# Optimization experiments

Hardware: AMD Instinct MI355X
Metric: run time of the kernel (lower is better)

Reference implementation:

```python
import jax, jax.numpy as jnp
import numpy as np
from jax import ops as jops

N = 20000          # nodes
E = 320000         # edges
IN_DIM = 16        # input_dim_features_extractor
HID = 64           # hidden_dim_features_extractor
HEADS = 4          # n_attention_heads
LAYERS = 2         # n_layers_features_extractor
NEG_SLOPE = 0.2    # DGL EGATConv leaky_relu slope


def setup_inputs() -> dict:
    key = jax.random.key(0)
    ks = jax.random.split(key, 16)
    s = lambda *sh: 1.0 / np.sqrt(sh[-2] if len(sh) >= 2 else sh[-1])
    inp = {
        "node_feat": jax.random.normal(ks[0], (N, IN_DIM), jnp.float32),
        "edge_feat": jax.random.normal(ks[1], (E, HID), jnp.float32),
        "src": jax.random.randint(ks[2], (E,), 0, N, jnp.int32),
        "dst": jax.random.randint(ks[3], (E,), 0, N, jnp.int32),
        # features_embedder (MLP n_layers=1 -> single Linear IN_DIM->HID)
        "W_embed": jax.random.normal(ks[4], (IN_DIM, HID), jnp.float32) * s(IN_DIM, HID),
        "b_embed": jnp.zeros((HID,), jnp.float32),
        # per-layer EGATConv params (stacked over layer dim)
        "W_ni": jax.random.normal(ks[5], (LAYERS, HID, HEADS * HID), jnp.float32) * s(HID, 1),
        "W_nj": jax.random.normal(ks[6], (LAYERS, HID, HEADS * HID), jnp.float32) * s(HID, 1),
        "W_fij": jax.random.normal(ks[7], (LAYERS, HID, HEADS * HID), jnp.float32) * s(HID, 1),
        "b_att": jnp.zeros((LAYERS, HEADS * HID), jnp.float32),
        "attn": jax.random.normal(ks[8], (LAYERS, HEADS, HID), jnp.float32) * s(HID),
        "W_node": jax.random.normal(ks[9], (LAYERS, HID, HEADS * HID), jnp.float32) * s(HID, 1),
        # per-layer MLP (n_layers=1 -> Linear HEADS*HID -> HID)
        "W_mlp": jax.random.normal(ks[10], (LAYERS, HEADS * HID, HID), jnp.float32) * s(HEADS * HID, 1),
        "b_mlp": jnp.zeros((LAYERS, HID), jnp.float32),
    }
    return inp


def _egat(h, f, src, dst, W_ni, W_nj, W_fij, b, attn, W_node):
    """DGL EGATConv: edge-feature attention + softmax-weighted aggregation."""
    # per-edge attention features: u_add_v + edge proj + bias
    f_ni = h @ W_ni                         # (N, H*D)
    f_nj = h @ W_nj                         # (N, H*D)
    f_fij = f @ W_fij                       # (E, H*D)
    f_out = f_ni[src] + f_nj[dst] + f_fij + b
    f_out = jax.nn.leaky_relu(f_out, NEG_SLOPE).reshape(E, HEADS, HID)
    e = jnp.einsum("ehd,hd->eh", f_out, attn)            # (E, H) logits
    # edge softmax over incoming edges of each dst node (numerically stable)
    m = jops.segment_max(e, dst, num_segments=N)          # (N, H)
    a = jnp.exp(e - m[dst])
    z = jops.segment_sum(a, dst, num_segments=N)          # (N, H)
    a = a / z[dst]
    # weighted message aggregation
    hn = (h @ W_node).reshape(N, HEADS, HID)
    msg = hn[src] * a[:, :, None]                         # (E, H, D)
    out = jops.segment_sum(msg, dst, num_segments=N)      # (N, H, D)
    return out


def reference(node_feat, edge_feat, src, dst, W_embed, b_embed,
              W_ni, W_nj, W_fij, b_att, attn, W_node, W_mlp, b_mlp):
    features_list = [node_feat]                 # layer_pooling='all'
    features = node_feat @ W_embed + b_embed    # features_embedder
    features_list.append(features)
    for L in range(LAYERS):
        h = _egat(features, edge_feat, src, dst,
                  W_ni[L], W_nj[L], W_fij[L], b_att[L], attn[L], W_node[L])
        new = h.reshape(N, HEADS * HID) @ W_mlp[L] + b_mlp[L]
        features = new + features               # residual
        features_list.append(features)
    return jnp.concatenate(features_list, axis=-1)   # (N, 16 + 3*64)
```

## Files before the change

kernel.cpp:

```cpp
#include <hip/hip_runtime.h>
#include <math.h>

#define NN 20000
#define NE 320000
#define IN_DIM 16
#define HID 64
#define HEADS 4
#define HD 256
#define OUTW 208
#define NEG 0.2f

typedef unsigned short u16;
typedef unsigned int u32;
typedef __attribute__((ext_vector_type(8))) short bf16x8;
typedef __attribute__((ext_vector_type(8))) unsigned short u16x8;
typedef __attribute__((ext_vector_type(4))) float f32x4;

__device__ __forceinline__ float b2f(u16 u) {
  union { u32 i; float f; } c; c.i = ((u32)u) << 16; return c.f;
}
__device__ __forceinline__ u16 f2b(float f) {
  union { float f; u32 i; } c; c.f = f;
  u32 r = (c.i + 0x7FFFu + ((c.i >> 16) & 1u)) >> 16;
  return (u16)r;
}

__global__ void k_embed_count(const float* __restrict__ nf, const float* __restrict__ We,
                              const float* __restrict__ be, float* __restrict__ feat,
                              float* __restrict__ out, const int* __restrict__ dst,
                              int* __restrict__ counts) {
  int bid = blockIdx.x;
  const int EB = (NN * 64) / 256;
  if (bid < EB) {
    int tid = bid * 256 + threadIdx.x;
    int n = tid >> 6, c = tid & 63;
    float acc = be[c];
#pragma unroll
    for (int k = 0; k < IN_DIM; ++k)
      acc += nf[n * IN_DIM + k] * We[k * HID + c];
    feat[n * HID + c] = acc;
    out[n * OUTW + 16 + c] = acc;
    if (c < IN_DIM) out[n * OUTW + c] = nf[n * IN_DIM + c];
  } else {
    int e = (bid - EB) * 256 + threadIdx.x;
    if (e < NE) atomicAdd(&counts[dst[e]], 1);
  }
}

__global__ void k_scan(const int* __restrict__ counts, int* __restrict__ rowptr,
                       int* __restrict__ cursor) {
  __shared__ int wsum[16];
  __shared__ int tot;
  int lane = threadIdx.x & 63, wid = threadIdx.x >> 6;
  int running = 0;
  if (threadIdx.x == 0) rowptr[0] = 0;
  for (int base = 0; base < NN; base += 1024) {
    int i = base + threadIdx.x;
    int x = (i < NN) ? counts[i] : 0;
    if (i < NN) cursor[i] = 0;
#pragma unroll
    for (int d = 1; d < 64; d <<= 1) {
      int t = __shfl_up(x, d);
      if (lane >= d) x += t;
    }
    if (lane == 63) wsum[wid] = x;
    __syncthreads();
    if (wid == 0) {
      int wv = (lane < 16) ? wsum[lane] : 0;
#pragma unroll
      for (int d = 1; d < 16; d <<= 1) {
        int t = __shfl_up(wv, d);
        if (lane >= d) wv += t;
      }
      if (lane < 16) wsum[lane] = wv;
      if (lane == 15) tot = wv;
    }
    __syncthreads();
    int wpre = (wid == 0) ? 0 : wsum[wid - 1];
    if (i < NN) rowptr[i + 1] = running + wpre + x;
    running += tot;
    __syncthreads();
  }
}

__global__ void k_scatter(const int* __restrict__ dst, const int* __restrict__ src,
                          const int* __restrict__ rowptr, int* __restrict__ cursor,
                          int* __restrict__ eidx, int* __restrict__ srcp,
                          int* __restrict__ dstp) {
  int e = blockIdx.x * blockDim.x + threadIdx.x;
  if (e >= NE) return;
  int d = dst[e];
  int pos = rowptr[d] + atomicAdd(&cursor[d], 1);
  eidx[pos] = e;
  srcp[pos] = src[e];
  dstp[pos] = d;
}

__global__ void k_permute_prepw(const float* __restrict__ ef, const int* __restrict__ eidx,
                                u16* __restrict__ efbp, const float* __restrict__ Wf,
                                u16* __restrict__ Wt0, u16* __restrict__ Wt1) {
  int bid = blockIdx.x;
  const int PB = (NE * 16) / 256;
  if (bid < PB) {
    int t = bid * 256 + threadIdx.x;
    int slot = t >> 4, c = (t & 15) * 4;
    int e = eidx[slot];
    float4 v = *reinterpret_cast<const float4*>(&ef[(size_t)e * HID + c]);
    ushort4 o;
    o.x = f2b(v.x); o.y = f2b(v.y); o.z = f2b(v.z); o.w = f2b(v.w);
    *reinterpret_cast<ushort4*>(&efbp[(size_t)slot * HID + c]) = o;
  } else {
    int r = (bid - PB) * 256 + threadIdx.x;
    int Lw = r >> 14;
    int idx = r & 16383;
    int nn2 = idx >> 6, kk2 = idx & 63;
    u16* WtL = Lw ? Wt1 : Wt0;
    WtL[nn2 * HID + kk2] = f2b(Wf[(size_t)Lw * HID * HD + kk2 * HD + nn2]);
  }
}

__global__ __launch_bounds__(256) void k_nodeproj(
    const float* __restrict__ feat, const float* __restrict__ Wni,
    const float* __restrict__ Wnj, const float* __restrict__ Wnd,
    const float* __restrict__ batt, u16* __restrict__ fni,
    u16* __restrict__ fnj, u16* __restrict__ hn) {
  __shared__ float hs[8 * HID];
  int n0 = blockIdx.x * 8;
  int c = threadIdx.x;
  for (int i = threadIdx.x; i < 8 * HID; i += 256)
    hs[i] = feat[(size_t)(n0 + (i >> 6)) * HID + (i & 63)];
  __syncthreads();
  float aI[8] = {0}, aJ[8] = {0}, aN[8] = {0};
  for (int k = 0; k < HID; ++k) {
    float wi = Wni[k * HD + c], wj = Wnj[k * HD + c], wn = Wnd[k * HD + c];
#pragma unroll
    for (int t = 0; t < 8; ++t) {
      float x = hs[t * HID + k];
      aI[t] += x * wi; aJ[t] += x * wj; aN[t] += x * wn;
    }
  }
  float b = batt[c];
#pragma unroll
  for (int t = 0; t < 8; ++t) {
    int n = n0 + t;
    fni[(size_t)n * HD + c] = f2b(aI[t] + b);
    fnj[(size_t)n * HD + c] = f2b(aJ[t]);
    hn[(size_t)n * HD + c]  = f2b(aN[t]);
  }
}

__global__ __launch_bounds__(256) void k_edgelogits(
    const u16* __restrict__ efbp, const int* __restrict__ srcp,
    const int* __restrict__ dstp, const u16* __restrict__ fni,
    const u16* __restrict__ fnj, const u16* __restrict__ Wt,
    const float* __restrict__ attnL, float* __restrict__ elog) {
  __shared__ float gb[HEADS][16][68];
  int h = threadIdx.x >> 6;
  int l = threadIdx.x & 63;
  int q = l >> 4;
  int n = l & 15;
  bf16x8 bfr[4][2];
#pragma unroll
  for (int nt = 0; nt < 4; ++nt)
#pragma unroll
    for (int kk = 0; kk < 2; ++kk)
      bfr[nt][kk] = *reinterpret_cast<const bf16x8*>(
          &Wt[(h * 64 + nt * 16 + n) * HID + kk * 32 + q * 8]);
  float at[4];
#pragma unroll
  for (int nt = 0; nt < 4; ++nt) at[nt] = attnL[h * 64 + nt * 16 + n];

#define COMMIT(av, bv)                                                \
  {                                                                   \
    _Pragma("unroll")                                                 \
    for (int p = 0; p < 4; ++p) {                                     \
      float4 g;                                                       \
      g.x = b2f(av[p].x) + b2f(bv[p].x);                              \
      g.y = b2f(av[p].y) + b2f(bv[p].y);                              \
      g.z = b2f(av[p].z) + b2f(bv[p].z);                              \
      g.w = b2f(av[p].w) + b2f(bv[p].w);                              \
      *reinterpret_cast<float4*>(&gb[h][p * 4 + q][4 * n]) = g;       \
    }                                                                 \
  }

#define TILEMMA(aa0, aa1, ibase)                                                  \
  {                                                                               \
    float sumr[4] = {0.f, 0.f, 0.f, 0.f};                                         \
    _Pragma("unroll")                                                             \
    for (int nt = 0; nt < 4; ++nt) {                                              \
      f32x4 acc = {0.f, 0.f, 0.f, 0.f};                                           \
      acc = __builtin_amdgcn_mfma_f32_16x16x32_bf16(aa0, bfr[nt][0], acc, 0, 0, 0); \
      acc = __builtin_amdgcn_mfma_f32_16x16x32_bf16(aa1, bfr[nt][1], acc, 0, 0, 0); \
      _Pragma("unroll")                                                           \
      for (int r = 0; r < 4; ++r) {                                               \
        float v = acc[r] + gb[h][q * 4 + r][nt * 16 + n];                         \
        v = v > 0.f ? v : NEG * v;                                                \
        sumr[r] += v * at[nt];                                                    \
      }                                                                           \
    }                                                                             \
    _Pragma("unroll")                                                             \
    for (int r = 0; r < 4; ++r) {                                                 \
      float v = sumr[r];                                                          \
      v += __shfl_xor(v, 1);                                                      \
      v += __shfl_xor(v, 2);                                                      \
      v += __shfl_xor(v, 4);                                                      \
      v += __shfl_xor(v, 8);                                                      \
      sumr[r] = v;                                                                \
    }                                                                             \
    if (n == 0) {                                                                 \
      float4 o_;                                                                  \
      o_.x = sumr[0]; o_.y = sumr[1]; o_.z = sumr[2]; o_.w = sumr[3];             \
      *reinterpret_cast<float4*>(&elog[(size_t)h * NE + (ibase) + q * 4]) = o_;   \
    }                                                                             \
  }

  const int NT = NE / 16;
  const int G = gridDim.x;
  for (int tile = blockIdx.x; tile < NT; tile += 2 * G) {
    int t1 = tile + G;
    int i0 = tile * 16;
    bf16x8 a00 = *reinterpret_cast<const bf16x8*>(&efbp[(size_t)(i0 + n) * HID + q * 8]);
    bf16x8 a01 = *reinterpret_cast<const bf16x8*>(&efbp[(size_t)(i0 + n) * HID + 32 + q * 8]);
    ushort4 av0[4], bv0[4];
#pragma unroll
    for (int p = 0; p < 4; ++p) {
      int i = i0 + p * 4 + q;
      int s = srcp[i], d = dstp[i];
      av0[p] = *reinterpret_cast<const ushort4*>(&fni[(size_t)s * HD + h * 64 + 4 * n]);
      bv0[p] = *reinterpret_cast<const ushort4*>(&fnj[(size_t)d * HD + h * 64 + 4 * n]);
    }
    int i1 = 0;
    bf16x8 a10 = {}, a11 = {};
    ushort4 av1[4], bv1[4];
    bool has1 = (t1 < NT);
    if (has1) {
      i1 = t1 * 16;
      a10 = *reinterpret_cast<const bf16x8*>(&efbp[(size_t)(i1 + n) * HID + q * 8]);
      a11 = *reinterpret_cast<const bf16x8*>(&efbp[(size_t)(i1 + n) * HID + 32 + q * 8]);
#pragma unroll
      for (int p = 0; p < 4; ++p) {
        int i = i1 + p * 4 + q;
        int s = srcp[i], d = dstp[i];
        av1[p] = *reinterpret_cast<const ushort4*>(&fni[(size_t)s * HD + h * 64 + 4 * n]);
        bv1[p] = *reinterpret_cast<const ushort4*>(&fnj[(size_t)d * HD + h * 64 + 4 * n]);
      }
    }
    COMMIT(av0, bv0);
    TILEMMA(a00, a01, i0);
    if (has1) {
      COMMIT(av1, bv1);
      TILEMMA(a10, a11, i1);
    }
  }
#undef COMMIT
#undef TILEMMA
}

__global__ __launch_bounds__(256) void k_agg(
    const int* __restrict__ rowptr, const int* __restrict__ srcp,
    const float* __restrict__ elog, const u16* __restrict__ hn,
    float* __restrict__ agg) {
  int n = (blockIdx.x * blockDim.x + threadIdx.x) >> 6;
  int j = threadIdx.x & 63;
  if (n >= NN) return;
  int s0 = rowptr[n], s1 = rowptr[n + 1];
  int half = j >> 5;
  int lo = j & 31;
  int hA = (j >> 3) & 3;
  int u = (j & 7) + 8 * half;
  const float* er = elog + (size_t)hA * NE;
  float m = -1e30f;
  for (int i = s0 + u; i < s1; i += 16) m = fmaxf(m, er[i]);
  m = fmaxf(m, __shfl_xor(m, 1));
  m = fmaxf(m, __shfl_xor(m, 2));
  m = fmaxf(m, __shfl_xor(m, 4));
  m = fmaxf(m, __shfl_xor(m, 32));
  float z = 0.f;
  for (int i = s0 + u; i < s1; i += 16) z += __expf(er[i] - m);
  z += __shfl_xor(z, 1);
  z += __shfl_xor(z, 2);
  z += __shfl_xor(z, 4);
  z += __shfl_xor(z, 32);
  float invz = (z > 0.f) ? 1.0f / z : 0.f;
  float a8[8] = {0.f, 0.f, 0.f, 0.f, 0.f, 0.f, 0.f, 0.f};
  int i = s0;
  for (; i + 8 <= s1; i += 8) {
    int sv[8]; float wv[8];
#pragma unroll
    for (int t = 0; t < 8; ++t) sv[t] = srcp[i + t];
#pragma unroll
    for (int t = 0; t < 8; ++t) wv[t] = __expf(er[i + t] - m) * invz;
    u16x8 vv[4];
#pragma unroll
    for (int g = 0; g < 4; ++g)
      vv[g] = *reinterpret_cast<const u16x8*>(&hn[(size_t)sv[2 * g + half] * HD + 8 * lo]);
#pragma unroll
    for (int g = 0; g < 4; ++g) {
      float w = wv[2 * g + half];
#pragma unroll
      for (int e = 0; e < 8; ++e) a8[e] += b2f(vv[g][e]) * w;
    }
  }
  for (; i < s1; ++i) {
    int s = srcp[i];
    float w = half ? 0.f : (__expf(er[i] - m) * invz);
    u16x8 v = *reinterpret_cast<const u16x8*>(&hn[(size_t)s * HD + 8 * lo]);
#pragma unroll
    for (int e = 0; e < 8; ++e) a8[e] += b2f(v[e]) * w;
  }
#pragma unroll
  for (int e = 0; e < 8; ++e) a8[e] += __shfl_xor(a8[e], 32);
  if (j < 32) {
    float4 o0, o1;
    o0.x = a8[0]; o0.y = a8[1]; o0.z = a8[2]; o0.w = a8[3];
    o1.x = a8[4]; o1.y = a8[5]; o1.z = a8[6]; o1.w = a8[7];
    *reinterpret_cast<float4*>(&agg[(size_t)n * HD + 8 * lo]) = o0;
    *reinterpret_cast<float4*>(&agg[(size_t)n * HD + 8 * lo + 4]) = o1;
  }
}

__global__ __launch_bounds__(256) void k_mlp(
    const float* __restrict__ agg, const float* __restrict__ Wm,
    const float* __restrict__ bm, float* __restrict__ feat,
    float* __restrict__ out, int outoff) {
  __shared__ float as_[32 * HD];
  int n0 = blockIdx.x * 32;
  for (int i = threadIdx.x; i < 32 * HD; i += 256) as_[i] = agg[(size_t)n0 * HD + i];
  __syncthreads();
  int c = threadIdx.x & 63;
  int g = threadIdx.x >> 6;
  float acc[8] = {0};
  for (int k = 0; k < HD; ++k) {
    float wv = Wm[k * HID + c];
#pragma unroll
    for (int t = 0; t < 8; ++t)
      acc[t] += as_[(g * 8 + t) * HD + k] * wv;
  }
  float b = bm[c];
#pragma unroll
  for (int t = 0; t < 8; ++t) {
    int n = n0 + g * 8 + t;
    float v = acc[t] + b + feat[n * HID + c];
    feat[n * HID + c] = v;
    out[n * OUTW + outoff + c] = v;
  }
}

extern "C" void kernel_launch(void* const* d_in, const int* in_sizes, int n_in,
                              void* d_out, int out_size, void* d_ws, size_t ws_size,
                              hipStream_t stream) {
  const float* node_feat = (const float*)d_in[0];
  const float* edge_feat = (const float*)d_in[1];
  const int*   src       = (const int*)d_in[2];
  const int*   dst       = (const int*)d_in[3];
  const float* W_embed   = (const float*)d_in[4];
  const float* b_embed   = (const float*)d_in[5];
  const float* W_ni      = (const float*)d_in[6];
  const float* W_nj      = (const float*)d_in[7];
  const float* W_fij     = (const float*)d_in[8];
  const float* b_att     = (const float*)d_in[9];
  const float* attn      = (const float*)d_in[10];
  const float* W_node    = (const float*)d_in[11];
  const float* W_mlp     = (const float*)d_in[12];
  const float* b_mlp     = (const float*)d_in[13];
  float* out = (float*)d_out;

  float* ws   = (float*)d_ws;
  float* feat = ws;
  u16*  fni   = (u16*)(feat + (size_t)NN * HID);
  u16*  fnj   = fni + (size_t)NN * HD;
  u16*  hn    = fnj + (size_t)NN * HD;
  u16*  efbp  = hn + (size_t)NN * HD;
  u16*  Wt0   = efbp + (size_t)NE * HID;
  u16*  Wt1   = Wt0 + (size_t)HD * HID;
  float* elog = (float*)(Wt1 + (size_t)HD * HID);
  int* counts = (int*)(elog + (size_t)NE * HEADS);
  int* rowptr = counts + NN;
  int* cursor = rowptr + NN + 1;
  int* eidx   = cursor + NN;
  int* srcp   = eidx + NE;
  int* dstp   = srcp + NE;
  float* aggb = (float*)fni;

  hipMemsetAsync(counts, 0, sizeof(int) * NN, stream);

  k_embed_count<<<(NN * 64) / 256 + NE / 256, 256, 0, stream>>>(
      node_feat, W_embed, b_embed, feat, out, dst, counts);
  k_scan<<<1, 1024, 0, stream>>>(counts, rowptr, cursor);
  k_scatter<<<NE / 256, 256, 0, stream>>>(dst, src, rowptr, cursor, eidx, srcp, dstp);
  k_permute_prepw<<<(NE * 16) / 256 + 128, 256, 0, stream>>>(
      edge_feat, eidx, efbp, W_fij, Wt0, Wt1);

  for (int L = 0; L < 2; ++L) {
    const float* WniL = W_ni + (size_t)L * HID * HD;
    const float* WnjL = W_nj + (size_t)L * HID * HD;
    const float* WndL = W_node + (size_t)L * HID * HD;
    const float* battL = b_att + (size_t)L * HD;
    const float* attnL = attn + (size_t)L * HEADS * HID;
    const float* WmL  = W_mlp + (size_t)L * HD * HID;
    const float* bmL  = b_mlp + (size_t)L * HID;
    u16* WtL = L ? Wt1 : Wt0;

    k_nodeproj<<<NN / 8, 256, 0, stream>>>(feat, WniL, WnjL, WndL, battL, fni, fnj, hn);
    k_edgelogits<<<2048, 256, 0, stream>>>(efbp, srcp, dstp, fni, fnj, WtL, attnL, elog);
    k_agg<<<(NN * 64) / 256, 256, 0, stream>>>(rowptr, srcp, elog, hn, aggb);
    k_mlp<<<NN / 32, 256, 0, stream>>>(aggb, WmL, bmL, feat, out, 80 + L * 64);
  }
}
```

Measured before the change: 529.6 us.

## Move node projections to split-bf16 MFMA and vectorize edge index loads

Replaces the scalar FP32 node projection kernel with an MFMA kernel that uses a hi/lo bf16 split of features and weights (three-product emulation) to keep near-FP32 accuracy. Split features are produced in the embed and MLP kernels, and split weights are prepared once in the prep kernel. The edge-logit kernel also loads src/dst indices as int4 vectors, reordering the shared-memory row mapping to match. This adds extra workspace and write traffic for the split buffers, and drops the lo*lo term, which costs a little precision.

```diff
diff --git a/kernel.cpp b/kernel.cpp
--- a/kernel.cpp
+++ b/kernel.cpp
@@ -27,6 +27,7 @@
 
 __global__ void k_embed_count(const float* __restrict__ nf, const float* __restrict__ We,
                               const float* __restrict__ be, float* __restrict__ feat,
+                              u16* __restrict__ fbH, u16* __restrict__ fbL,
                               float* __restrict__ out, const int* __restrict__ dst,
                               int* __restrict__ counts) {
   int bid = blockIdx.x;
@@ -39,6 +40,9 @@
     for (int k = 0; k < IN_DIM; ++k)
       acc += nf[n * IN_DIM + k] * We[k * HID + c];
     feat[n * HID + c] = acc;
+    u16 hi = f2b(acc);
+    fbH[n * HID + c] = hi;
+    fbL[n * HID + c] = f2b(acc - b2f(hi));
     out[n * OUTW + 16 + c] = acc;
     if (c < IN_DIM) out[n * OUTW + c] = nf[n * IN_DIM + c];
   } else {
@@ -98,7 +102,9 @@
 
 __global__ void k_permute_prepw(const float* __restrict__ ef, const int* __restrict__ eidx,
                                 u16* __restrict__ efbp, const float* __restrict__ Wf,
-                                u16* __restrict__ Wt0, u16* __restrict__ Wt1) {
+                                u16* __restrict__ Wt0, u16* __restrict__ Wt1,
+                                const float* __restrict__ Wni, const float* __restrict__ Wnj,
+                                const float* __restrict__ Wnd, u16* __restrict__ wsp) {
   int bid = blockIdx.x;
   const int PB = (NE * 16) / 256;
   if (bid < PB) {
@@ -111,41 +117,71 @@
     *reinterpret_cast<ushort4*>(&efbp[(size_t)slot * HID + c]) = o;
   } else {
     int r = (bid - PB) * 256 + threadIdx.x;
-    int Lw = r >> 14;
-    int idx = r & 16383;
-    int nn2 = idx >> 6, kk2 = idx & 63;
-    u16* WtL = Lw ? Wt1 : Wt0;
-    WtL[nn2 * HID + kk2] = f2b(Wf[(size_t)Lw * HID * HD + kk2 * HD + nn2]);
-  }
-}
-
-__global__ __launch_bounds__(256) void k_nodeproj(
-    const float* __restrict__ feat, const float* __restrict__ Wni,
-    const float* __restrict__ Wnj, const float* __restrict__ Wnd,
+    if (r < 32768) {
+      int Lw = r >> 14;
+      int idx = r & 16383;
+      int nn2 = idx >> 6, kk2 = idx & 63;
+      u16* WtL = Lw ? Wt1 : Wt0;
+      WtL[nn2 * HID + kk2] = f2b(Wf[(size_t)Lw * HID * HD + kk2 * HD + nn2]);
+    } else {
+      int r2 = r - 32768;
+      int m = r2 >> 15;
+      int rem = r2 & 32767;
+      int L = rem >> 14;
+      int idx = rem & 16383;
+      int n = idx >> 6, k = idx & 63;
+      const float* W = (m == 0) ? Wni : (m == 1) ? Wnj : Wnd;
+      float w = W[(size_t)L * HID * HD + k * HD + n];
+      u16 hi = f2b(w);
+      u16 lo = f2b(w - b2f(hi));
+      size_t base = (size_t)((L * 3 + m) * 2) * 16384;
+      wsp[base + idx] = hi;
+      wsp[base + 16384 + idx] = lo;
+    }
+  }
+}
+
+__global__ __launch_bounds__(256) void k_nodeproj_mfma(
+    const u16* __restrict__ fbH, const u16* __restrict__ fbL,
+    const u16* __restrict__ wspL,
     const float* __restrict__ batt, u16* __restrict__ fni,
     u16* __restrict__ fnj, u16* __restrict__ hn) {
-  __shared__ float hs[8 * HID];
-  int n0 = blockIdx.x * 8;
-  int c = threadIdx.x;
-  for (int i = threadIdx.x; i < 8 * HID; i += 256)
-    hs[i] = feat[(size_t)(n0 + (i >> 6)) * HID + (i & 63)];
-  __syncthreads();
-  float aI[8] = {0}, aJ[8] = {0}, aN[8] = {0};
-  for (int k = 0; k < HID; ++k) {
-    float wi = Wni[k * HD + c], wj = Wnj[k * HD + c], wn = Wnd[k * HD + c];
-#pragma unroll
-    for (int t = 0; t < 8; ++t) {
-      float x = hs[t * HID + k];
-      aI[t] += x * wi; aJ[t] += x * wj; aN[t] += x * wn;
-    }
-  }
-  float b = batt[c];
-#pragma unroll
-  for (int t = 0; t < 8; ++t) {
-    int n = n0 + t;
-    fni[(size_t)n * HD + c] = f2b(aI[t] + b);
-    fnj[(size_t)n * HD + c] = f2b(aJ[t]);
-    hn[(size_t)n * HD + c]  = f2b(aN[t]);
+  int n0 = blockIdx.x * 16;
+  int w = threadIdx.x >> 6;
+  int l = threadIdx.x & 63;
+  int q = l >> 4, n = l & 15;
+  const size_t abase = (size_t)(n0 + n) * HID + q * 8;
+  bf16x8 aH0 = *reinterpret_cast<const bf16x8*>(&fbH[abase]);
+  bf16x8 aH1 = *reinterpret_cast<const bf16x8*>(&fbH[abase + 32]);
+  bf16x8 aL0 = *reinterpret_cast<const bf16x8*>(&fbL[abase]);
+  bf16x8 aL1 = *reinterpret_cast<const bf16x8*>(&fbL[abase + 32]);
+#pragma unroll
+  for (int nt = 0; nt < 12; ++nt) {
+    int ct = w * 192 + nt * 16;
+    int m = ct >> 8;
+    int lc = ct & 255;
+    const u16* BH = wspL + (size_t)(m * 2) * 16384;
+    const u16* BL = BH + 16384;
+    size_t bbase = (size_t)(lc + n) * HID + q * 8;
+    bf16x8 bH0 = *reinterpret_cast<const bf16x8*>(&BH[bbase]);
+    bf16x8 bH1 = *reinterpret_cast<const bf16x8*>(&BH[bbase + 32]);
+    bf16x8 bL0 = *reinterpret_cast<const bf16x8*>(&BL[bbase]);
+    bf16x8 bL1 = *reinterpret_cast<const bf16x8*>(&BL[bbase + 32]);
+    f32x4 acc = {0.f, 0.f, 0.f, 0.f};
+    acc = __builtin_amdgcn_mfma_f32_16x16x32_bf16(aH0, bH0, acc, 0, 0, 0);
+    acc = __builtin_amdgcn_mfma_f32_16x16x32_bf16(aH1, bH1, acc, 0, 0, 0);
+    acc = __builtin_amdgcn_mfma_f32_16x16x32_bf16(aH0, bL0, acc, 0, 0, 0);
+    acc = __builtin_amdgcn_mfma_f32_16x16x32_bf16(aH1, bL1, acc, 0, 0, 0);
+    acc = __builtin_amdgcn_mfma_f32_16x16x32_bf16(aL0, bH0, acc, 0, 0, 0);
+    acc = __builtin_amdgcn_mfma_f32_16x16x32_bf16(aL1, bH1, acc, 0, 0, 0);
+    float badd = 0.f;
+    if (m == 0) badd = batt[lc + n];
+    u16* dstm = (m == 0) ? fni : (m == 1) ? fnj : hn;
+#pragma unroll
+    for (int r = 0; r < 4; ++r) {
+      int node = n0 + q * 4 + r;
+      dstm[(size_t)node * HD + lc + n] = f2b(acc[r] + badd);
+    }
   }
 }
 
@@ -170,6 +206,20 @@
 #pragma unroll
   for (int nt = 0; nt < 4; ++nt) at[nt] = attnL[h * 64 + nt * 16 + n];
 
+#define GATHER(sv, dv, av, bv)                                                    \
+  {                                                                               \
+    int s0_ = sv.x, d0_ = dv.x, s1_ = sv.y, d1_ = dv.y;                           \
+    int s2_ = sv.z, d2_ = dv.z, s3_ = sv.w, d3_ = dv.w;                           \
+    av[0] = *reinterpret_cast<const ushort4*>(&fni[(size_t)s0_ * HD + h * 64 + 4 * n]); \
+    bv[0] = *reinterpret_cast<const ushort4*>(&fnj[(size_t)d0_ * HD + h * 64 + 4 * n]); \
+    av[1] = *reinterpret_cast<const ushort4*>(&fni[(size_t)s1_ * HD + h * 64 + 4 * n]); \
+    bv[1] = *reinterpret_cast<const ushort4*>(&fnj[(size_t)d1_ * HD + h * 64 + 4 * n]); \
+    av[2] = *reinterpret_cast<const ushort4*>(&fni[(size_t)s2_ * HD + h * 64 + 4 * n]); \
+    bv[2] = *reinterpret_cast<const ushort4*>(&fnj[(size_t)d2_ * HD + h * 64 + 4 * n]); \
+    av[3] = *reinterpret_cast<const ushort4*>(&fni[(size_t)s3_ * HD + h * 64 + 4 * n]); \
+    bv[3] = *reinterpret_cast<const ushort4*>(&fnj[(size_t)d3_ * HD + h * 64 + 4 * n]); \
+  }
+
 #define COMMIT(av, bv)                                                \
   {                                                                   \
     _Pragma("unroll")                                                 \
@@ -179,7 +229,7 @@
       g.y = b2f(av[p].y) + b2f(bv[p].y);                              \
       g.z = b2f(av[p].z) + b2f(bv[p].z);                              \
       g.w = b2f(av[p].w) + b2f(bv[p].w);                              \
-      *reinterpret_cast<float4*>(&gb[h][p * 4 + q][4 * n]) = g;       \
+      *reinterpret_cast<float4*>(&gb[h][4 * q + p][4 * n]) = g;       \
     }                                                                 \
   }
 
@@ -221,14 +271,10 @@
     int i0 = tile * 16;
     bf16x8 a00 = *reinterpret_cast<const bf16x8*>(&efbp[(size_t)(i0 + n) * HID + q * 8]);
     bf16x8 a01 = *reinterpret_cast<const bf16x8*>(&efbp[(size_t)(i0 + n) * HID + 32 + q * 8]);
+    int4 sv0 = *reinterpret_cast<const int4*>(&srcp[i0 + 4 * q]);
+    int4 dv0 = *reinterpret_cast<const int4*>(&dstp[i0 + 4 * q]);
     ushort4 av0[4], bv0[4];
-#pragma unroll
-    for (int p = 0; p < 4; ++p) {
-      int i = i0 + p * 4 + q;
-      int s = srcp[i], d = dstp[i];
-      av0[p] = *reinterpret_cast<const ushort4*>(&fni[(size_t)s * HD + h * 64 + 4 * n]);
-      bv0[p] = *reinterpret_cast<const ushort4*>(&fnj[(size_t)d * HD + h * 64 + 4 * n]);
-    }
+    GATHER(sv0, dv0, av0, bv0);
     int i1 = 0;
     bf16x8 a10 = {}, a11 = {};
     ushort4 av1[4], bv1[4];
@@ -237,13 +283,9 @@
       i1 = t1 * 16;
       a10 = *reinterpret_cast<const bf16x8*>(&efbp[(size_t)(i1 + n) * HID + q * 8]);
       a11 = *reinterpret_cast<const bf16x8*>(&efbp[(size_t)(i1 + n) * HID + 32 + q * 8]);
-#pragma unroll
-      for (int p = 0; p < 4; ++p) {
-        int i = i1 + p * 4 + q;
-        int s = srcp[i], d = dstp[i];
-        av1[p] = *reinterpret_cast<const ushort4*>(&fni[(size_t)s * HD + h * 64 + 4 * n]);
-        bv1[p] = *reinterpret_cast<const ushort4*>(&fnj[(size_t)d * HD + h * 64 + 4 * n]);
-      }
+      int4 sv1 = *reinterpret_cast<const int4*>(&srcp[i1 + 4 * q]);
+      int4 dv1 = *reinterpret_cast<const int4*>(&dstp[i1 + 4 * q]);
+      GATHER(sv1, dv1, av1, bv1);
     }
     COMMIT(av0, bv0);
     TILEMMA(a00, a01, i0);
@@ -252,6 +294,7 @@
       TILEMMA(a10, a11, i1);
     }
   }
+#undef GATHER
 #undef COMMIT
 #undef TILEMMA
 }
@@ -322,6 +365,7 @@
 __global__ __launch_bounds__(256) void k_mlp(
     const float* __restrict__ agg, const float* __restrict__ Wm,
     const float* __restrict__ bm, float* __restrict__ feat,
+    u16* __restrict__ fbH, u16* __restrict__ fbL,
     float* __restrict__ out, int outoff) {
   __shared__ float as_[32 * HD];
   int n0 = blockIdx.x * 32;
@@ -342,6 +386,9 @@
     int n = n0 + g * 8 + t;
     float v = acc[t] + b + feat[n * HID + c];
     feat[n * HID + c] = v;
+    u16 hi = f2b(v);
+    fbH[n * HID + c] = hi;
+    fbL[n * HID + c] = f2b(v - b2f(hi));
     out[n * OUTW + outoff + c] = v;
   }
 }
@@ -373,37 +420,38 @@
   u16*  efbp  = hn + (size_t)NN * HD;
   u16*  Wt0   = efbp + (size_t)NE * HID;
   u16*  Wt1   = Wt0 + (size_t)HD * HID;
-  float* elog = (float*)(Wt1 + (size_t)HD * HID);
+  u16*  wsp   = Wt1 + (size_t)HD * HID;
+  float* elog = (float*)(wsp + 12 * 16384);
   int* counts = (int*)(elog + (size_t)NE * HEADS);
   int* rowptr = counts + NN;
   int* cursor = rowptr + NN + 1;
   int* eidx   = cursor + NN;
   int* srcp   = eidx + NE;
   int* dstp   = srcp + NE;
+  u16* fbH    = (u16*)(dstp + NE);
+  u16* fbL    = fbH + (size_t)NN * HID;
   float* aggb = (float*)fni;
 
   hipMemsetAsync(counts, 0, sizeof(int) * NN, stream);
 
   k_embed_count<<<(NN * 64) / 256 + NE / 256, 256, 0, stream>>>(
-      node_feat, W_embed, b_embed, feat, out, dst, counts);
+      node_feat, W_embed, b_embed, feat, fbH, fbL, out, dst, counts);
   k_scan<<<1, 1024, 0, stream>>>(counts, rowptr, cursor);
   k_scatter<<<NE / 256, 256, 0, stream>>>(dst, src, rowptr, cursor, eidx, srcp, dstp);
-  k_permute_prepw<<<(NE * 16) / 256 + 128, 256, 0, stream>>>(
-      edge_feat, eidx, efbp, W_fij, Wt0, Wt1);
+  k_permute_prepw<<<(NE * 16) / 256 + 512, 256, 0, stream>>>(
+      edge_feat, eidx, efbp, W_fij, Wt0, Wt1, W_ni, W_nj, W_node, wsp);
 
   for (int L = 0; L < 2; ++L) {
-    const float* WniL = W_ni + (size_t)L * HID * HD;
-    const float* WnjL = W_nj + (size_t)L * HID * HD;
-    const float* WndL = W_node + (size_t)L * HID * HD;
     const float* battL = b_att + (size_t)L * HD;
     const float* attnL = attn + (size_t)L * HEADS * HID;
     const float* WmL  = W_mlp + (size_t)L * HD * HID;
     const float* bmL  = b_mlp + (size_t)L * HID;
     u16* WtL = L ? Wt1 : Wt0;
-
-    k_nodeproj<<<NN / 8, 256, 0, stream>>>(feat, WniL, WnjL, WndL, battL, fni, fnj, hn);
+    u16* wspL = wsp + (size_t)(L * 3 * 2) * 16384;
+
+    k_nodeproj_mfma<<<NN / 16, 256, 0, stream>>>(fbH, fbL, wspL, battL, fni, fnj, hn);
     k_edgelogits<<<2048, 256, 0, stream>>>(efbp, srcp, dstp, fni, fnj, WtL, attnL, elog);
     k_agg<<<(NN * 64) / 256, 256, 0, stream>>>(rowptr, srcp, elog, hn, aggb);
-    k_mlp<<<NN / 32, 256, 0, stream>>>(aggb, WmL, bmL, feat, out, 80 + L * 64);
-  }
-}
+    k_mlp<<<NN / 32, 256, 0, stream>>>(aggb, WmL, bmL, feat, fbH, fbL, out, 80 + L * 64);
+  }
+}
```

After: 541.0 us. 2.2% more time.
